# Performance work log

Hardware: AMD Instinct MI355X
Metric: run time of the kernel (lower is better)

Reference implementation:

```python
import jax, jax.numpy as jnp
import numpy as np

EPS = 1e-5


def _rms_norm(x, w):
    # x: [..., C], w: [C]
    inv = jax.lax.rsqrt(jnp.mean(x * x, axis=-1, keepdims=True) + EPS)
    return x * inv * w


def setup_inputs() -> dict:
    key = jax.random.key(0)
    ks = jax.random.split(key, 8)
    N, H, C = 16384, 16, 32
    NE = 196608
    return {
        "q": jax.random.normal(ks[0], (N, H, C), dtype=jnp.float32),
        "k": jax.random.normal(ks[1], (N, H, C), dtype=jnp.float32),
        "v": jax.random.normal(ks[2], (N, H, C), dtype=jnp.float32),
        "e": jax.random.normal(ks[3], (NE, H, C), dtype=jnp.float32),
        "w_q_norm": jnp.ones((C,), dtype=jnp.float32),
        "w_k_norm": jnp.ones((C,), dtype=jnp.float32),
        "edge_src": jax.random.randint(ks[4], (NE,), 0, N, dtype=jnp.int32),
        "edge_dst": jax.random.randint(ks[5], (NE,), 0, N, dtype=jnp.int32),
    }


def reference(q, k, v, e, w_q_norm, w_k_norm, edge_src, edge_dst):
    N, H, C = q.shape
    qk_scale = 1.0 / np.sqrt(float(C))
    # fused QK RMSNorm (qk_norm == 1, elementwise_affine)
    qn = _rms_norm(q, w_q_norm)            # [N,H,C]
    kn = _rms_norm(k, w_k_norm)            # [N,H,C]
    ke = kn[edge_src] + e                  # [NE,H,C]
    ve = v[edge_src] + e                   # [NE,H,C]
    s = jnp.einsum("ehc,ehc->eh", qn[edge_dst], ke) * qk_scale  # [NE,H]
    # segment softmax over incoming edges per dst node
    m = jax.ops.segment_max(s, edge_dst, num_segments=N)        # [N,H]
    m = jnp.where(jnp.isfinite(m), m, 0.0)                      # empty rows -> 0 (matches kernel)
    alpha = jnp.exp(s - m[edge_dst])                            # [NE,H]
    denom = jax.ops.segment_sum(alpha, edge_dst, num_segments=N)            # [N,H]
    num = jax.ops.segment_sum(alpha[..., None] * ve, edge_dst, num_segments=N)  # [N,H,C]
    out = num / jnp.where(denom > 0, denom, 1.0)[..., None]
    return out
```

## Files before the change

kernel.cpp:

```cpp
#include <hip/hip_runtime.h>
#include <math.h>

#define H_DIM 16
#define C_DIM 32
#define HC_DIM (H_DIM * C_DIM)
#define EPSF 1e-5f

__device__ __forceinline__ float reduce8(float x) {
    x += __shfl_xor(x, 1);
    x += __shfl_xor(x, 2);
    x += __shfl_xor(x, 4);
    return x;
}

typedef float f4_raw __attribute__((ext_vector_type(4)));
__device__ __forceinline__ float4 nt_load4(const float* p) {
    f4_raw r = __builtin_nontemporal_load((const f4_raw*)p);
    return make_float4(r.x, r.y, r.z, r.w);
}
__device__ __forceinline__ void nt_store4(float* p, float4 v) {
    f4_raw r = {v.x, v.y, v.z, v.w};
    __builtin_nontemporal_store(r, (f4_raw*)p);
}

__global__ void zero_kernel(int* __restrict__ p, int n) {
    int i = blockIdx.x * blockDim.x + threadIdx.x;
    if (i < n) p[i] = 0;
}

__global__ __launch_bounds__(256)
void hist_kinv_kernel(const int* __restrict__ edst, int* __restrict__ counts,
                      const float* __restrict__ k, float* __restrict__ kinv,
                      int ne, int rows, int histBlocks) {
    if ((int)blockIdx.x < histBlocks) {
        int i4 = (blockIdx.x * 256 + threadIdx.x) * 4;
        if (i4 + 4 <= ne) {
            int4 d = *(const int4*)(edst + i4);
            atomicAdd(&counts[d.x], 1);
            atomicAdd(&counts[d.y], 1);
            atomicAdd(&counts[d.z], 1);
            atomicAdd(&counts[d.w], 1);
        } else {
            for (int j = i4; j < ne; ++j) atomicAdd(&counts[edst[j]], 1);
        }
    } else {
        int gt = (blockIdx.x - histBlocks) * 256 + threadIdx.x;
        int row = gt >> 3;
        if (row < rows) {
            const float4 kv = *(const float4*)(k + (size_t)row * C_DIM + ((gt & 7) << 2));
            float s = kv.x * kv.x + kv.y * kv.y + kv.z * kv.z + kv.w * kv.w;
            s = reduce8(s);
            if ((gt & 7) == 0) kinv[row] = rsqrtf(s * (1.0f / C_DIM) + EPSF);
        }
    }
}

__global__ __launch_bounds__(1024)
void scan_kernel(const int* __restrict__ counts, int* __restrict__ offsets, int n) {
    __shared__ int wsum[16];
    __shared__ int carry_s;
    const int tid = threadIdx.x;
    const int lane = tid & 63;
    const int wid = tid >> 6;
    if (tid == 0) carry_s = 0;
    __syncthreads();
    for (int b0 = 0; b0 < n; b0 += 16384) {
        const int base = b0 + tid * 16;
        int c[16];
        if (base + 16 <= n) {
            const int4* p = (const int4*)(counts + base);
            int4 t0 = p[0], t1 = p[1], t2 = p[2], t3 = p[3];
            c[0]=t0.x; c[1]=t0.y; c[2]=t0.z; c[3]=t0.w;
            c[4]=t1.x; c[5]=t1.y; c[6]=t1.z; c[7]=t1.w;
            c[8]=t2.x; c[9]=t2.y; c[10]=t2.z; c[11]=t2.w;
            c[12]=t3.x; c[13]=t3.y; c[14]=t3.z; c[15]=t3.w;
        } else {
            #pragma unroll
            for (int j = 0; j < 16; ++j) c[j] = (base + j < n) ? counts[base + j] : 0;
        }
        int s = 0;
        #pragma unroll
        for (int j = 0; j < 16; ++j) s += c[j];
        int v = s;
        #pragma unroll
        for (int off = 1; off < 64; off <<= 1) {
            int y = __shfl_up(v, off);
            if (lane >= off) v += y;
        }
        if (lane == 63) wsum[wid] = v;
        __syncthreads();
        if (wid == 0 && lane < 16) {
            int w = wsum[lane];
            #pragma unroll
            for (int off = 1; off < 16; off <<= 1) {
                int y = __shfl_up(w, off);
                if (lane >= off) w += y;
            }
            wsum[lane] = w;
        }
        __syncthreads();
        const int carry = carry_s;
        int p = carry + (wid ? wsum[wid - 1] : 0) + (v - s);
        int o[16];
        #pragma unroll
        for (int j = 0; j < 16; ++j) { o[j] = p; p += c[j]; }
        if (base + 16 <= n) {
            int4* q = (int4*)(offsets + base);
            q[0] = make_int4(o[0], o[1], o[2], o[3]);
            q[1] = make_int4(o[4], o[5], o[6], o[7]);
            q[2] = make_int4(o[8], o[9], o[10], o[11]);
            q[3] = make_int4(o[12], o[13], o[14], o[15]);
        } else {
            #pragma unroll
            for (int j = 0; j < 16; ++j)
                if (base + j < n) offsets[base + j] = o[j];
        }
        if (n - 1 >= base && n - 1 < base + 16) offsets[n] = p;
        __syncthreads();
        if (tid == 0) carry_s = carry + wsum[15];
        __syncthreads();
    }
}

__global__ void scatter_kernel(const int* __restrict__ esrc, const int* __restrict__ edst,
                               const int* __restrict__ offsets, int* __restrict__ cursor,
                               int2* __restrict__ perm, int ne) {
    int i4 = (blockIdx.x * blockDim.x + threadIdx.x) * 4;
    if (i4 + 4 <= ne) {
        int4 d = *(const int4*)(edst + i4);
        int4 s = *(const int4*)(esrc + i4);
        int p0 = offsets[d.x] + atomicAdd(&cursor[d.x], 1);
        perm[p0] = make_int2(s.x, i4 + 0);
        int p1 = offsets[d.y] + atomicAdd(&cursor[d.y], 1);
        perm[p1] = make_int2(s.y, i4 + 1);
        int p2 = offsets[d.z] + atomicAdd(&cursor[d.z], 1);
        perm[p2] = make_int2(s.z, i4 + 2);
        int p3 = offsets[d.w] + atomicAdd(&cursor[d.w], 1);
        perm[p3] = make_int2(s.w, i4 + 3);
    } else {
        for (int j = i4; j < ne; ++j) {
            int d = edst[j];
            int pos = offsets[d] + atomicAdd(&cursor[d], 1);
            perm[pos] = make_int2(esrc[j], j);
        }
    }
}

struct EdgeData {
    float4 ev, kv, vv;
    float  ki;
};

__device__ __forceinline__ EdgeData load_edge(int2 p,
                                              const float* __restrict__ e,
                                              const float* __restrict__ k,
                                              const float* __restrict__ v,
                                              const float* __restrict__ kinv,
                                              int hc, int h) {
    EdgeData d;
    d.ev = nt_load4(e + (size_t)p.y * HC_DIM + hc);
    d.kv = *(const float4*)(k + p.x * HC_DIM + hc);
    d.vv = *(const float4*)(v + p.x * HC_DIM + hc);
    d.ki = kinv[p.x * H_DIM + h];
    return d;
}

__device__ __forceinline__ void update_edge(const EdgeData& d,
                                            float4 qnw, float4 qns,
                                            float& m, float& l, float4& acc) {
    float dk = qnw.x * d.kv.x + qnw.y * d.kv.y + qnw.z * d.kv.z + qnw.w * d.kv.w;
    float de = qns.x * d.ev.x + qns.y * d.ev.y + qns.z * d.ev.z + qns.w * d.ev.w;
    float s = reduce8(dk * d.ki + de);
    float mnew = fmaxf(m, s);
    float sc = __expf(m - mnew);
    float al = __expf(s - mnew);
    l = l * sc + al;
    acc.x = acc.x * sc + al * (d.vv.x + d.ev.x);
    acc.y = acc.y * sc + al * (d.vv.y + d.ev.y);
    acc.z = acc.z * sc + al * (d.vv.z + d.ev.z);
    acc.w = acc.w * sc + al * (d.vv.w + d.ev.w);
    m = mnew;
}

__global__ __launch_bounds__(128, 4)
void attn_kernel(const float* __restrict__ q, const float* __restrict__ k,
                 const float* __restrict__ v, const float* __restrict__ e,
                 const float* __restrict__ wq, const float* __restrict__ wk,
                 const float* __restrict__ kinv,
                 const int* __restrict__ offsets, const int2* __restrict__ perm,
                 float* __restrict__ out)
{
    const int node = blockIdx.x;
    const int t = threadIdx.x;
    const int hc = t << 2;
    const int c4 = (t & 7) << 2;
    const int h  = t >> 3;
    const float qk_scale = 0.17677669529663687f;

    const int node_off = node * HC_DIM + hc;

    float4 qv = nt_load4(q + node_off);
    float qs = qv.x * qv.x + qv.y * qv.y + qv.z * qv.z + qv.w * qv.w;
    qs = reduce8(qs);
    float qinv = rsqrtf(qs * (1.0f / C_DIM) + EPSF);
    float4 wqv = *(const float4*)(wq + c4);
    float4 wkv = *(const float4*)(wk + c4);
    float4 qn = make_float4(qv.x * qinv * wqv.x, qv.y * qinv * wqv.y,
                            qv.z * qinv * wqv.z, qv.w * qinv * wqv.w);
    float4 qnw = make_float4(qn.x * wkv.x * qk_scale, qn.y * wkv.y * qk_scale,
                             qn.z * wkv.z * qk_scale, qn.w * wkv.w * qk_scale);
    float4 qns = make_float4(qn.x * qk_scale, qn.y * qk_scale,
                             qn.z * qk_scale, qn.w * qk_scale);

    const int row0 = offsets[node];
    const int row1 = offsets[node + 1];
    const int len = row1 - row0;
    const int mid = row0 + ((len + 1) >> 1);

    float mA = -INFINITY, lA = 0.0f, mB = -INFINITY, lB = 0.0f;
    float4 accA = make_float4(0.f, 0.f, 0.f, 0.f);
    float4 accB = make_float4(0.f, 0.f, 0.f, 0.f);

    int jA = row0, jB = mid;
    if (jB < row1) {
        int2 pA = perm[jA];
        int2 pB = perm[jB];
        EdgeData a = load_edge(pA, e, k, v, kinv, hc, h);
        EdgeData b = load_edge(pB, e, k, v, kinv, hc, h);
        ++jA; ++jB;
        bool haveNext = (jB < row1);
        int2 nA, nB;
        if (haveNext) { nA = perm[jA]; nB = perm[jB]; }
        while (haveNext) {
            EdgeData a2 = load_edge(nA, e, k, v, kinv, hc, h);
            EdgeData b2 = load_edge(nB, e, k, v, kinv, hc, h);
            ++jA; ++jB;
            haveNext = (jB < row1);
            if (haveNext) { nA = perm[jA]; nB = perm[jB]; }
            update_edge(a, qnw, qns, mA, lA, accA);
            update_edge(b, qnw, qns, mB, lB, accB);
            a = a2; b = b2;
        }
        update_edge(a, qnw, qns, mA, lA, accA);
        update_edge(b, qnw, qns, mB, lB, accB);
    }
    while (jA < mid) {
        int2 p = perm[jA];
        EdgeData a = load_edge(p, e, k, v, kinv, hc, h);
        update_edge(a, qnw, qns, mA, lA, accA);
        ++jA;
    }

    float M = fmaxf(mA, mB);
    float fA = (lA > 0.0f) ? __expf(mA - M) : 0.0f;
    float fB = (lB > 0.0f) ? __expf(mB - M) : 0.0f;
    float l = lA * fA + lB * fB;
    float4 acc = make_float4(accA.x * fA + accB.x * fB,
                             accA.y * fA + accB.y * fB,
                             accA.z * fA + accB.z * fB,
                             accA.w * fA + accB.w * fB);

    float invl = (l > 0.0f) ? (1.0f / l) : 0.0f;
    nt_store4(out + node_off, make_float4(acc.x * invl, acc.y * invl,
                                          acc.z * invl, acc.w * invl));
}

extern "C" void kernel_launch(void* const* d_in, const int* in_sizes, int n_in,
                              void* d_out, int out_size, void* d_ws, size_t ws_size,
                              hipStream_t stream) {
    const float* q  = (const float*)d_in[0];
    const float* k  = (const float*)d_in[1];
    const float* v  = (const float*)d_in[2];
    const float* e  = (const float*)d_in[3];
    const float* wq = (const float*)d_in[4];
    const float* wk = (const float*)d_in[5];
    const int* esrc = (const int*)d_in[6];
    const int* edst = (const int*)d_in[7];
    float* out = (float*)d_out;

    const int NE = in_sizes[6];
    const int HC = in_sizes[3] / NE;
    const int N  = in_sizes[0] / HC;

    int2* perm    = (int2*)d_ws;
    int* counts   = (int*)(perm + NE);
    int* cursor   = counts + N;
    int* offsets  = cursor + N;
    float* kinv   = (float*)(offsets + N + 1);

    const int rows = N * H_DIM;
    const int histBlocks = (NE / 4 + 255) / 256;
    const int kinvBlocks = (rows * 8 + 255) / 256;
    const int scatBlocks = (NE / 4 + 255) / 256;

    zero_kernel<<<(2 * N + 255) / 256, 256, 0, stream>>>(counts, 2 * N);
    hist_kinv_kernel<<<histBlocks + kinvBlocks, 256, 0, stream>>>(edst, counts, k, kinv,
                                                                  NE, rows, histBlocks);
    scan_kernel<<<1, 1024, 0, stream>>>(counts, offsets, N);
    scatter_kernel<<<scatBlocks, 256, 0, stream>>>(esrc, edst, offsets, cursor,
                                                   perm, NE);
    attn_kernel<<<N, 128, 0, stream>>>(q, k, v, e, wq, wk, kinv, offsets, perm, out);
}
```

Measured before the change: 685.9 us.

## Split fused online-softmax attention into edge-parallel score and node value passes

The prep kernel now writes normalized, scaled Q and normalized K buffers. A new edge-parallel score kernel computes per-edge, per-head logits in edge order and stores them to a score buffer. A node-parallel value kernel then computes the max and sum per head from these scores, with 8 lanes splitting the edges, and accumulates the weighted values without online rescaling. This removes the serial online-softmax dependency and the gathered K loads from the per-node loop. In exchange it reads e twice, writes and reads extra Q, K and score buffers, and needs more workspace.

```diff
diff --git a/kernel.cpp b/kernel.cpp
--- a/kernel.cpp
+++ b/kernel.cpp
@@ -5,6 +5,7 @@
 #define C_DIM 32
 #define HC_DIM (H_DIM * C_DIM)
 #define EPSF 1e-5f
+#define QK_SCALE 0.17677669529663687f
 
 __device__ __forceinline__ float reduce8(float x) {
     x += __shfl_xor(x, 1);
@@ -12,6 +13,12 @@
     x += __shfl_xor(x, 4);
     return x;
 }
+__device__ __forceinline__ float reduce8_max(float x) {
+    x = fmaxf(x, __shfl_xor(x, 1));
+    x = fmaxf(x, __shfl_xor(x, 2));
+    x = fmaxf(x, __shfl_xor(x, 4));
+    return x;
+}
 
 typedef float f4_raw __attribute__((ext_vector_type(4)));
 __device__ __forceinline__ float4 nt_load4(const float* p) {
@@ -29,11 +36,14 @@
 }
 
 __global__ __launch_bounds__(256)
-void hist_kinv_kernel(const int* __restrict__ edst, int* __restrict__ counts,
-                      const float* __restrict__ k, float* __restrict__ kinv,
-                      int ne, int rows, int histBlocks) {
-    if ((int)blockIdx.x < histBlocks) {
-        int i4 = (blockIdx.x * 256 + threadIdx.x) * 4;
+void prep_kernel(const int* __restrict__ edst, int* __restrict__ counts,
+                 const float* __restrict__ q, const float* __restrict__ k,
+                 const float* __restrict__ wq, const float* __restrict__ wk,
+                 float* __restrict__ qns, float* __restrict__ knw,
+                 int ne, int rows, int histBlocks, int qkBlocks) {
+    int b = blockIdx.x;
+    if (b < histBlocks) {
+        int i4 = (b * 256 + threadIdx.x) * 4;
         if (i4 + 4 <= ne) {
             int4 d = *(const int4*)(edst + i4);
             atomicAdd(&counts[d.x], 1);
@@ -43,15 +53,31 @@
         } else {
             for (int j = i4; j < ne; ++j) atomicAdd(&counts[edst[j]], 1);
         }
+        return;
+    }
+    b -= histBlocks;
+    const bool isQ = (b < qkBlocks);
+    if (!isQ) b -= qkBlocks;
+    int gt = b * 256 + threadIdx.x;
+    int row = gt >> 3;
+    if (row >= rows) return;
+    const int c4 = (gt & 7) << 2;
+    const size_t off = (size_t)row * C_DIM + c4;
+    const float* src = isQ ? q : k;
+    float4 x = *(const float4*)(src + off);
+    float ss = x.x * x.x + x.y * x.y + x.z * x.z + x.w * x.w;
+    ss = reduce8(ss);
+    float inv = rsqrtf(ss * (1.0f / C_DIM) + EPSF);
+    if (isQ) {
+        float4 w = *(const float4*)(wq + c4);
+        *(float4*)(qns + off) = make_float4(x.x * inv * w.x * QK_SCALE,
+                                            x.y * inv * w.y * QK_SCALE,
+                                            x.z * inv * w.z * QK_SCALE,
+                                            x.w * inv * w.w * QK_SCALE);
     } else {
-        int gt = (blockIdx.x - histBlocks) * 256 + threadIdx.x;
-        int row = gt >> 3;
-        if (row < rows) {
-            const float4 kv = *(const float4*)(k + (size_t)row * C_DIM + ((gt & 7) << 2));
-            float s = kv.x * kv.x + kv.y * kv.y + kv.z * kv.z + kv.w * kv.w;
-            s = reduce8(s);
-            if ((gt & 7) == 0) kinv[row] = rsqrtf(s * (1.0f / C_DIM) + EPSF);
-        }
+        float4 w = *(const float4*)(wk + c4);
+        *(float4*)(knw + off) = make_float4(x.x * inv * w.x, x.y * inv * w.y,
+                                            x.z * inv * w.z, x.w * inv * w.w);
     }
 }
 
@@ -105,11 +131,11 @@
         #pragma unroll
         for (int j = 0; j < 16; ++j) { o[j] = p; p += c[j]; }
         if (base + 16 <= n) {
-            int4* q = (int4*)(offsets + base);
-            q[0] = make_int4(o[0], o[1], o[2], o[3]);
-            q[1] = make_int4(o[4], o[5], o[6], o[7]);
-            q[2] = make_int4(o[8], o[9], o[10], o[11]);
-            q[3] = make_int4(o[12], o[13], o[14], o[15]);
+            int4* qo = (int4*)(offsets + base);
+            qo[0] = make_int4(o[0], o[1], o[2], o[3]);
+            qo[1] = make_int4(o[4], o[5], o[6], o[7]);
+            qo[2] = make_int4(o[8], o[9], o[10], o[11]);
+            qo[3] = make_int4(o[12], o[13], o[14], o[15]);
         } else {
             #pragma unroll
             for (int j = 0; j < 16; ++j)
@@ -146,121 +172,83 @@
     }
 }
 
-struct EdgeData {
-    float4 ev, kv, vv;
-    float  ki;
-};
-
-__device__ __forceinline__ EdgeData load_edge(int2 p,
-                                              const float* __restrict__ e,
-                                              const float* __restrict__ k,
-                                              const float* __restrict__ v,
-                                              const float* __restrict__ kinv,
-                                              int hc, int h) {
-    EdgeData d;
-    d.ev = nt_load4(e + (size_t)p.y * HC_DIM + hc);
-    d.kv = *(const float4*)(k + p.x * HC_DIM + hc);
-    d.vv = *(const float4*)(v + p.x * HC_DIM + hc);
-    d.ki = kinv[p.x * H_DIM + h];
-    return d;
-}
-
-__device__ __forceinline__ void update_edge(const EdgeData& d,
-                                            float4 qnw, float4 qns,
-                                            float& m, float& l, float4& acc) {
-    float dk = qnw.x * d.kv.x + qnw.y * d.kv.y + qnw.z * d.kv.z + qnw.w * d.kv.w;
-    float de = qns.x * d.ev.x + qns.y * d.ev.y + qns.z * d.ev.z + qns.w * d.ev.w;
-    float s = reduce8(dk * d.ki + de);
-    float mnew = fmaxf(m, s);
-    float sc = __expf(m - mnew);
-    float al = __expf(s - mnew);
-    l = l * sc + al;
-    acc.x = acc.x * sc + al * (d.vv.x + d.ev.x);
-    acc.y = acc.y * sc + al * (d.vv.y + d.ev.y);
-    acc.z = acc.z * sc + al * (d.vv.z + d.ev.z);
-    acc.w = acc.w * sc + al * (d.vv.w + d.ev.w);
-    m = mnew;
-}
-
-__global__ __launch_bounds__(128, 4)
-void attn_kernel(const float* __restrict__ q, const float* __restrict__ k,
-                 const float* __restrict__ v, const float* __restrict__ e,
-                 const float* __restrict__ wq, const float* __restrict__ wk,
-                 const float* __restrict__ kinv,
-                 const int* __restrict__ offsets, const int2* __restrict__ perm,
-                 float* __restrict__ out)
+__global__ __launch_bounds__(256, 8)
+void score_kernel(const float* __restrict__ qns, const float* __restrict__ knw,
+                  const float* __restrict__ e,
+                  const int* __restrict__ esrc, const int* __restrict__ edst,
+                  float* __restrict__ sbuf, int ne) {
+    const int t = threadIdx.x;
+    const int eid = blockIdx.x * 2 + (t >> 7);
+    if (eid >= ne) return;
+    const int tt = t & 127;
+    const int hc = tt << 2;
+    const int h = tt >> 3;
+    const int src = esrc[eid];
+    const int dst = edst[eid];
+    const float4 ev = nt_load4(e + (size_t)eid * HC_DIM + hc);
+    const float4 kv = *(const float4*)(knw + (size_t)src * HC_DIM + hc);
+    const float4 qv = *(const float4*)(qns + (size_t)dst * HC_DIM + hc);
+    float d = qv.x * (kv.x + ev.x) + qv.y * (kv.y + ev.y)
+            + qv.z * (kv.z + ev.z) + qv.w * (kv.w + ev.w);
+    d = reduce8(d);
+    if ((tt & 7) == 0) sbuf[(size_t)eid * H_DIM + h] = d;
+}
+
+__global__ __launch_bounds__(128, 8)
+void value_kernel(const float* __restrict__ v, const float* __restrict__ e,
+                  const float* __restrict__ sbuf,
+                  const int* __restrict__ offsets, const int2* __restrict__ perm,
+                  float* __restrict__ out)
 {
     const int node = blockIdx.x;
     const int t = threadIdx.x;
     const int hc = t << 2;
-    const int c4 = (t & 7) << 2;
-    const int h  = t >> 3;
-    const float qk_scale = 0.17677669529663687f;
-
+    const int h = t >> 3;
+    const int lane8 = t & 7;
     const int node_off = node * HC_DIM + hc;
-
-    float4 qv = nt_load4(q + node_off);
-    float qs = qv.x * qv.x + qv.y * qv.y + qv.z * qv.z + qv.w * qv.w;
-    qs = reduce8(qs);
-    float qinv = rsqrtf(qs * (1.0f / C_DIM) + EPSF);
-    float4 wqv = *(const float4*)(wq + c4);
-    float4 wkv = *(const float4*)(wk + c4);
-    float4 qn = make_float4(qv.x * qinv * wqv.x, qv.y * qinv * wqv.y,
-                            qv.z * qinv * wqv.z, qv.w * qinv * wqv.w);
-    float4 qnw = make_float4(qn.x * wkv.x * qk_scale, qn.y * wkv.y * qk_scale,
-                             qn.z * wkv.z * qk_scale, qn.w * wkv.w * qk_scale);
-    float4 qns = make_float4(qn.x * qk_scale, qn.y * qk_scale,
-                             qn.z * qk_scale, qn.w * qk_scale);
 
     const int row0 = offsets[node];
     const int row1 = offsets[node + 1];
-    const int len = row1 - row0;
-    const int mid = row0 + ((len + 1) >> 1);
-
-    float mA = -INFINITY, lA = 0.0f, mB = -INFINITY, lB = 0.0f;
-    float4 accA = make_float4(0.f, 0.f, 0.f, 0.f);
-    float4 accB = make_float4(0.f, 0.f, 0.f, 0.f);
-
-    int jA = row0, jB = mid;
-    if (jB < row1) {
-        int2 pA = perm[jA];
-        int2 pB = perm[jB];
-        EdgeData a = load_edge(pA, e, k, v, kinv, hc, h);
-        EdgeData b = load_edge(pB, e, k, v, kinv, hc, h);
-        ++jA; ++jB;
-        bool haveNext = (jB < row1);
-        int2 nA, nB;
-        if (haveNext) { nA = perm[jA]; nB = perm[jB]; }
-        while (haveNext) {
-            EdgeData a2 = load_edge(nA, e, k, v, kinv, hc, h);
-            EdgeData b2 = load_edge(nB, e, k, v, kinv, hc, h);
-            ++jA; ++jB;
-            haveNext = (jB < row1);
-            if (haveNext) { nA = perm[jA]; nB = perm[jB]; }
-            update_edge(a, qnw, qns, mA, lA, accA);
-            update_edge(b, qnw, qns, mB, lB, accB);
-            a = a2; b = b2;
-        }
-        update_edge(a, qnw, qns, mA, lA, accA);
-        update_edge(b, qnw, qns, mB, lB, accB);
-    }
-    while (jA < mid) {
-        int2 p = perm[jA];
-        EdgeData a = load_edge(p, e, k, v, kinv, hc, h);
-        update_edge(a, qnw, qns, mA, lA, accA);
-        ++jA;
-    }
-
-    float M = fmaxf(mA, mB);
-    float fA = (lA > 0.0f) ? __expf(mA - M) : 0.0f;
-    float fB = (lB > 0.0f) ? __expf(mB - M) : 0.0f;
-    float l = lA * fA + lB * fB;
-    float4 acc = make_float4(accA.x * fA + accB.x * fB,
-                             accA.y * fA + accB.y * fB,
-                             accA.z * fA + accB.z * fB,
-                             accA.w * fA + accB.w * fB);
-
-    float invl = (l > 0.0f) ? (1.0f / l) : 0.0f;
+    if (row0 >= row1) {
+        nt_store4(out + node_off, make_float4(0.f, 0.f, 0.f, 0.f));
+        return;
+    }
+
+    float mr = -INFINITY, lr = 0.0f;
+    for (int j = row0 + lane8; j < row1; j += 8) {
+        float sv = sbuf[(size_t)perm[j].y * H_DIM + h];
+        float mn = fmaxf(mr, sv);
+        lr = lr * __expf(mr - mn) + __expf(sv - mn);
+        mr = mn;
+    }
+    const float M = reduce8_max(mr);
+    float lc = (lr > 0.0f) ? lr * __expf(mr - M) : 0.0f;
+    const float l = reduce8(lc);
+    const float invl = 1.0f / l;
+
+    float4 acc = make_float4(0.f, 0.f, 0.f, 0.f);
+    int2 p = perm[row0];
+    float4 ev = nt_load4(e + (size_t)p.y * HC_DIM + hc);
+    float4 vv = *(const float4*)(v + (size_t)p.x * HC_DIM + hc);
+    float sv = sbuf[(size_t)p.y * H_DIM + h];
+    for (int j = row0; j + 1 < row1; ++j) {
+        int2 p1 = perm[j + 1];
+        float4 ev1 = nt_load4(e + (size_t)p1.y * HC_DIM + hc);
+        float4 vv1 = *(const float4*)(v + (size_t)p1.x * HC_DIM + hc);
+        float sv1 = sbuf[(size_t)p1.y * H_DIM + h];
+        float al = __expf(sv - M);
+        acc.x += al * (vv.x + ev.x);
+        acc.y += al * (vv.y + ev.y);
+        acc.z += al * (vv.z + ev.z);
+        acc.w += al * (vv.w + ev.w);
+        ev = ev1; vv = vv1; sv = sv1;
+    }
+    float al = __expf(sv - M);
+    acc.x += al * (vv.x + ev.x);
+    acc.y += al * (vv.y + ev.y);
+    acc.z += al * (vv.z + ev.z);
+    acc.w += al * (vv.w + ev.w);
+
     nt_store4(out + node_off, make_float4(acc.x * invl, acc.y * invl,
                                           acc.z * invl, acc.w * invl));
 }
@@ -282,22 +270,25 @@
     const int HC = in_sizes[3] / NE;
     const int N  = in_sizes[0] / HC;
 
-    int2* perm    = (int2*)d_ws;
-    int* counts   = (int*)(perm + NE);
-    int* cursor   = counts + N;
-    int* offsets  = cursor + N;
-    float* kinv   = (float*)(offsets + N + 1);
+    char* wsp = (char*)d_ws;
+    int2*  perm = (int2*)wsp;                 wsp += (size_t)NE * sizeof(int2);
+    float* qns  = (float*)wsp;                wsp += (size_t)N * HC_DIM * sizeof(float);
+    float* knw  = (float*)wsp;                wsp += (size_t)N * HC_DIM * sizeof(float);
+    float* sbuf = (float*)wsp;                wsp += (size_t)NE * H_DIM * sizeof(float);
+    int* counts  = (int*)wsp;
+    int* cursor  = counts + N;
+    int* offsets = cursor + N;
 
     const int rows = N * H_DIM;
     const int histBlocks = (NE / 4 + 255) / 256;
-    const int kinvBlocks = (rows * 8 + 255) / 256;
-    const int scatBlocks = (NE / 4 + 255) / 256;
+    const int qkBlocks   = (rows * 8 + 255) / 256;
 
     zero_kernel<<<(2 * N + 255) / 256, 256, 0, stream>>>(counts, 2 * N);
-    hist_kinv_kernel<<<histBlocks + kinvBlocks, 256, 0, stream>>>(edst, counts, k, kinv,
-                                                                  NE, rows, histBlocks);
+    prep_kernel<<<histBlocks + 2 * qkBlocks, 256, 0, stream>>>(
+        edst, counts, q, k, wq, wk, qns, knw, NE, rows, histBlocks, qkBlocks);
     scan_kernel<<<1, 1024, 0, stream>>>(counts, offsets, N);
-    scatter_kernel<<<scatBlocks, 256, 0, stream>>>(esrc, edst, offsets, cursor,
-                                                   perm, NE);
-    attn_kernel<<<N, 128, 0, stream>>>(q, k, v, e, wq, wk, kinv, offsets, perm, out);
-}
+    scatter_kernel<<<(NE / 4 + 255) / 256, 256, 0, stream>>>(esrc, edst, offsets, cursor,
+                                                             perm, NE);
+    score_kernel<<<(NE + 1) / 2, 256, 0, stream>>>(qns, knw, e, esrc, edst, sbuf, NE);
+    value_kernel<<<N, 128, 0, stream>>>(v, e, sbuf, offsets, perm, out);
+}
```

New measurement: 800.2 us. 1.17x slower.

## Bucket edges by source within each destination and prenormalize K

Applied to the files above, without the earlier changes.

The CSR sort key changes from destination alone to destination times eight coarse source-range buckets. Each node's edges are then visited in roughly ascending source order, so gathers of k and v hit more nearby addresses and reuse L2. K is also normalized and weighted once in the prep kernel and written to a workspace buffer, so the attention inner loop needs one fused dot product and no kinv gather. In exchange, the scan grows eightfold over a single-block kernel, and writing the full normalized K tensor costs extra bandwidth.

```diff
diff --git a/kernel.cpp b/kernel.cpp
--- a/kernel.cpp
+++ b/kernel.cpp
@@ -5,6 +5,8 @@
 #define C_DIM 32
 #define HC_DIM (H_DIM * C_DIM)
 #define EPSF 1e-5f
+#define QK_SCALE 0.17677669529663687f
+#define NBUCK 8
 
 __device__ __forceinline__ float reduce8(float x) {
     x += __shfl_xor(x, 1);
@@ -29,30 +31,39 @@
 }
 
 __global__ __launch_bounds__(256)
-void hist_kinv_kernel(const int* __restrict__ edst, int* __restrict__ counts,
-                      const float* __restrict__ k, float* __restrict__ kinv,
-                      int ne, int rows, int histBlocks) {
-    if ((int)blockIdx.x < histBlocks) {
-        int i4 = (blockIdx.x * 256 + threadIdx.x) * 4;
+void prep_kernel(const int* __restrict__ esrc, const int* __restrict__ edst,
+                 int* __restrict__ counts,
+                 const float* __restrict__ k, const float* __restrict__ wk,
+                 float* __restrict__ knw,
+                 int ne, int rows, int histBlocks, int bshift) {
+    int b = blockIdx.x;
+    if (b < histBlocks) {
+        int i4 = (b * 256 + threadIdx.x) * 4;
         if (i4 + 4 <= ne) {
             int4 d = *(const int4*)(edst + i4);
-            atomicAdd(&counts[d.x], 1);
-            atomicAdd(&counts[d.y], 1);
-            atomicAdd(&counts[d.z], 1);
-            atomicAdd(&counts[d.w], 1);
+            int4 s = *(const int4*)(esrc + i4);
+            atomicAdd(&counts[d.x * NBUCK + (s.x >> bshift)], 1);
+            atomicAdd(&counts[d.y * NBUCK + (s.y >> bshift)], 1);
+            atomicAdd(&counts[d.z * NBUCK + (s.z >> bshift)], 1);
+            atomicAdd(&counts[d.w * NBUCK + (s.w >> bshift)], 1);
         } else {
-            for (int j = i4; j < ne; ++j) atomicAdd(&counts[edst[j]], 1);
-        }
-    } else {
-        int gt = (blockIdx.x - histBlocks) * 256 + threadIdx.x;
-        int row = gt >> 3;
-        if (row < rows) {
-            const float4 kv = *(const float4*)(k + (size_t)row * C_DIM + ((gt & 7) << 2));
-            float s = kv.x * kv.x + kv.y * kv.y + kv.z * kv.z + kv.w * kv.w;
-            s = reduce8(s);
-            if ((gt & 7) == 0) kinv[row] = rsqrtf(s * (1.0f / C_DIM) + EPSF);
-        }
-    }
+            for (int j = i4; j < ne; ++j)
+                atomicAdd(&counts[edst[j] * NBUCK + (esrc[j] >> bshift)], 1);
+        }
+        return;
+    }
+    int gt = (b - histBlocks) * 256 + threadIdx.x;
+    int row = gt >> 3;
+    if (row >= rows) return;
+    const int c4 = (gt & 7) << 2;
+    const size_t off = (size_t)row * C_DIM + c4;
+    float4 x = *(const float4*)(k + off);
+    float ss = x.x * x.x + x.y * x.y + x.z * x.z + x.w * x.w;
+    ss = reduce8(ss);
+    float inv = rsqrtf(ss * (1.0f / C_DIM) + EPSF);
+    float4 w = *(const float4*)(wk + c4);
+    *(float4*)(knw + off) = make_float4(x.x * inv * w.x, x.y * inv * w.y,
+                                        x.z * inv * w.z, x.w * inv * w.w);
 }
 
 __global__ __launch_bounds__(1024)
@@ -105,11 +116,11 @@
         #pragma unroll
         for (int j = 0; j < 16; ++j) { o[j] = p; p += c[j]; }
         if (base + 16 <= n) {
-            int4* q = (int4*)(offsets + base);
-            q[0] = make_int4(o[0], o[1], o[2], o[3]);
-            q[1] = make_int4(o[4], o[5], o[6], o[7]);
-            q[2] = make_int4(o[8], o[9], o[10], o[11]);
-            q[3] = make_int4(o[12], o[13], o[14], o[15]);
+            int4* qo = (int4*)(offsets + base);
+            qo[0] = make_int4(o[0], o[1], o[2], o[3]);
+            qo[1] = make_int4(o[4], o[5], o[6], o[7]);
+            qo[2] = make_int4(o[8], o[9], o[10], o[11]);
+            qo[3] = make_int4(o[12], o[13], o[14], o[15]);
         } else {
             #pragma unroll
             for (int j = 0; j < 16; ++j)
@@ -122,25 +133,30 @@
     }
 }
 
-__global__ void scatter_kernel(const int* __restrict__ esrc, const int* __restrict__ edst,
-                               const int* __restrict__ offsets, int* __restrict__ cursor,
-                               int2* __restrict__ perm, int ne) {
+__global__ __launch_bounds__(256)
+void scatter_kernel(const int* __restrict__ esrc, const int* __restrict__ edst,
+                    const int* __restrict__ offsets, int* __restrict__ cursor,
+                    int2* __restrict__ perm, int ne, int bshift) {
     int i4 = (blockIdx.x * blockDim.x + threadIdx.x) * 4;
     if (i4 + 4 <= ne) {
         int4 d = *(const int4*)(edst + i4);
         int4 s = *(const int4*)(esrc + i4);
-        int p0 = offsets[d.x] + atomicAdd(&cursor[d.x], 1);
+        int k0 = d.x * NBUCK + (s.x >> bshift);
+        int p0 = offsets[k0] + atomicAdd(&cursor[k0], 1);
         perm[p0] = make_int2(s.x, i4 + 0);
-        int p1 = offsets[d.y] + atomicAdd(&cursor[d.y], 1);
+        int k1 = d.y * NBUCK + (s.y >> bshift);
+        int p1 = offsets[k1] + atomicAdd(&cursor[k1], 1);
         perm[p1] = make_int2(s.y, i4 + 1);
-        int p2 = offsets[d.z] + atomicAdd(&cursor[d.z], 1);
+        int k2 = d.z * NBUCK + (s.z >> bshift);
+        int p2 = offsets[k2] + atomicAdd(&cursor[k2], 1);
         perm[p2] = make_int2(s.z, i4 + 2);
-        int p3 = offsets[d.w] + atomicAdd(&cursor[d.w], 1);
+        int k3 = d.w * NBUCK + (s.w >> bshift);
+        int p3 = offsets[k3] + atomicAdd(&cursor[k3], 1);
         perm[p3] = make_int2(s.w, i4 + 3);
     } else {
         for (int j = i4; j < ne; ++j) {
-            int d = edst[j];
-            int pos = offsets[d] + atomicAdd(&cursor[d], 1);
+            int kk = edst[j] * NBUCK + (esrc[j] >> bshift);
+            int pos = offsets[kk] + atomicAdd(&cursor[kk], 1);
             perm[pos] = make_int2(esrc[j], j);
         }
     }
@@ -148,29 +164,25 @@
 
 struct EdgeData {
     float4 ev, kv, vv;
-    float  ki;
 };
 
 __device__ __forceinline__ EdgeData load_edge(int2 p,
                                               const float* __restrict__ e,
-                                              const float* __restrict__ k,
+                                              const float* __restrict__ knw,
                                               const float* __restrict__ v,
-                                              const float* __restrict__ kinv,
-                                              int hc, int h) {
+                                              int hc) {
     EdgeData d;
     d.ev = nt_load4(e + (size_t)p.y * HC_DIM + hc);
-    d.kv = *(const float4*)(k + p.x * HC_DIM + hc);
-    d.vv = *(const float4*)(v + p.x * HC_DIM + hc);
-    d.ki = kinv[p.x * H_DIM + h];
+    d.kv = *(const float4*)(knw + (size_t)p.x * HC_DIM + hc);
+    d.vv = *(const float4*)(v + (size_t)p.x * HC_DIM + hc);
     return d;
 }
 
-__device__ __forceinline__ void update_edge(const EdgeData& d,
-                                            float4 qnw, float4 qns,
+__device__ __forceinline__ void update_edge(const EdgeData& d, float4 qns,
                                             float& m, float& l, float4& acc) {
-    float dk = qnw.x * d.kv.x + qnw.y * d.kv.y + qnw.z * d.kv.z + qnw.w * d.kv.w;
-    float de = qns.x * d.ev.x + qns.y * d.ev.y + qns.z * d.ev.z + qns.w * d.ev.w;
-    float s = reduce8(dk * d.ki + de);
+    float dd = qns.x * (d.kv.x + d.ev.x) + qns.y * (d.kv.y + d.ev.y)
+             + qns.z * (d.kv.z + d.ev.z) + qns.w * (d.kv.w + d.ev.w);
+    float s = reduce8(dd);
     float mnew = fmaxf(m, s);
     float sc = __expf(m - mnew);
     float al = __expf(s - mnew);
@@ -183,10 +195,9 @@
 }
 
 __global__ __launch_bounds__(128, 4)
-void attn_kernel(const float* __restrict__ q, const float* __restrict__ k,
+void attn_kernel(const float* __restrict__ q, const float* __restrict__ knw,
                  const float* __restrict__ v, const float* __restrict__ e,
-                 const float* __restrict__ wq, const float* __restrict__ wk,
-                 const float* __restrict__ kinv,
+                 const float* __restrict__ wq,
                  const int* __restrict__ offsets, const int2* __restrict__ perm,
                  float* __restrict__ out)
 {
@@ -194,26 +205,18 @@
     const int t = threadIdx.x;
     const int hc = t << 2;
     const int c4 = (t & 7) << 2;
-    const int h  = t >> 3;
-    const float qk_scale = 0.17677669529663687f;
-
     const int node_off = node * HC_DIM + hc;
 
     float4 qv = nt_load4(q + node_off);
     float qs = qv.x * qv.x + qv.y * qv.y + qv.z * qv.z + qv.w * qv.w;
     qs = reduce8(qs);
-    float qinv = rsqrtf(qs * (1.0f / C_DIM) + EPSF);
+    float qinv = rsqrtf(qs * (1.0f / C_DIM) + EPSF) * QK_SCALE;
     float4 wqv = *(const float4*)(wq + c4);
-    float4 wkv = *(const float4*)(wk + c4);
-    float4 qn = make_float4(qv.x * qinv * wqv.x, qv.y * qinv * wqv.y,
-                            qv.z * qinv * wqv.z, qv.w * qinv * wqv.w);
-    float4 qnw = make_float4(qn.x * wkv.x * qk_scale, qn.y * wkv.y * qk_scale,
-                             qn.z * wkv.z * qk_scale, qn.w * wkv.w * qk_scale);
-    float4 qns = make_float4(qn.x * qk_scale, qn.y * qk_scale,
-                             qn.z * qk_scale, qn.w * qk_scale);
-
-    const int row0 = offsets[node];
-    const int row1 = offsets[node + 1];
+    float4 qns = make_float4(qv.x * qinv * wqv.x, qv.y * qinv * wqv.y,
+                             qv.z * qinv * wqv.z, qv.w * qinv * wqv.w);
+
+    const int row0 = offsets[node * NBUCK];
+    const int row1 = offsets[node * NBUCK + NBUCK];
     const int len = row1 - row0;
     const int mid = row0 + ((len + 1) >> 1);
 
@@ -225,29 +228,29 @@
     if (jB < row1) {
         int2 pA = perm[jA];
         int2 pB = perm[jB];
-        EdgeData a = load_edge(pA, e, k, v, kinv, hc, h);
-        EdgeData b = load_edge(pB, e, k, v, kinv, hc, h);
+        EdgeData a = load_edge(pA, e, knw, v, hc);
+        EdgeData b = load_edge(pB, e, knw, v, hc);
         ++jA; ++jB;
         bool haveNext = (jB < row1);
         int2 nA, nB;
         if (haveNext) { nA = perm[jA]; nB = perm[jB]; }
         while (haveNext) {
-            EdgeData a2 = load_edge(nA, e, k, v, kinv, hc, h);
-            EdgeData b2 = load_edge(nB, e, k, v, kinv, hc, h);
+            EdgeData a2 = load_edge(nA, e, knw, v, hc);
+            EdgeData b2 = load_edge(nB, e, knw, v, hc);
             ++jA; ++jB;
             haveNext = (jB < row1);
             if (haveNext) { nA = perm[jA]; nB = perm[jB]; }
-            update_edge(a, qnw, qns, mA, lA, accA);
-            update_edge(b, qnw, qns, mB, lB, accB);
+            update_edge(a, qns, mA, lA, accA);
+            update_edge(b, qns, mB, lB, accB);
             a = a2; b = b2;
         }
-        update_edge(a, qnw, qns, mA, lA, accA);
-        update_edge(b, qnw, qns, mB, lB, accB);
+        update_edge(a, qns, mA, lA, accA);
+        update_edge(b, qns, mB, lB, accB);
     }
     while (jA < mid) {
         int2 p = perm[jA];
-        EdgeData a = load_edge(p, e, k, v, kinv, hc, h);
-        update_edge(a, qnw, qns, mA, lA, accA);
+        EdgeData a = load_edge(p, e, knw, v, hc);
+        update_edge(a, qns, mA, lA, accA);
         ++jA;
     }
 
@@ -282,22 +285,27 @@
     const int HC = in_sizes[3] / NE;
     const int N  = in_sizes[0] / HC;
 
-    int2* perm    = (int2*)d_ws;
-    int* counts   = (int*)(perm + NE);
-    int* cursor   = counts + N;
-    int* offsets  = cursor + N;
-    float* kinv   = (float*)(offsets + N + 1);
+    int bshift = 0;
+    while ((NBUCK << bshift) < N) ++bshift;
+
+    const int NB = N * NBUCK;
+
+    char* wsp = (char*)d_ws;
+    int2*  perm = (int2*)wsp;   wsp += (size_t)NE * sizeof(int2);
+    float* knw  = (float*)wsp;  wsp += (size_t)N * HC_DIM * sizeof(float);
+    int* counts  = (int*)wsp;
+    int* cursor  = counts + NB;
+    int* offsets = cursor + NB;
 
     const int rows = N * H_DIM;
     const int histBlocks = (NE / 4 + 255) / 256;
-    const int kinvBlocks = (rows * 8 + 255) / 256;
-    const int scatBlocks = (NE / 4 + 255) / 256;
-
-    zero_kernel<<<(2 * N + 255) / 256, 256, 0, stream>>>(counts, 2 * N);
-    hist_kinv_kernel<<<histBlocks + kinvBlocks, 256, 0, stream>>>(edst, counts, k, kinv,
-                                                                  NE, rows, histBlocks);
-    scan_kernel<<<1, 1024, 0, stream>>>(counts, offsets, N);
-    scatter_kernel<<<scatBlocks, 256, 0, stream>>>(esrc, edst, offsets, cursor,
-                                                   perm, NE);
-    attn_kernel<<<N, 128, 0, stream>>>(q, k, v, e, wq, wk, kinv, offsets, perm, out);
-}
+    const int knwBlocks  = (rows * 8 + 255) / 256;
+
+    zero_kernel<<<(2 * NB + 255) / 256, 256, 0, stream>>>(counts, 2 * NB);
+    prep_kernel<<<histBlocks + knwBlocks, 256, 0, stream>>>(
+        esrc, edst, counts, k, wk, knw, NE, rows, histBlocks, bshift);
+    scan_kernel<<<1, 1024, 0, stream>>>(counts, offsets, NB);
+    scatter_kernel<<<(NE / 4 + 255) / 256, 256, 0, stream>>>(esrc, edst, offsets, cursor,
+                                                             perm, NE, bshift);
+    attn_kernel<<<N, 128, 0, stream>>>(q, knw, v, e, wq, offsets, perm, out);
+}
```

New measurement: 706.3 us. 1.03x slower.
